# Kernel tuning notes

Hardware: AMD Instinct MI355X
Metric: run time of the kernel (lower is better)

The kernel has to match this reference:

```python
import jax, jax.numpy as jnp
import numpy as np
import math

NQ = 8            # n_qubits (hardcoded in _TransformerBlockQuantum)
DIM = 2 ** NQ     # statevector size = 256
H = 16            # num_heads
EPS = 1e-5        # LayerNorm eps

# PauliZ expectation table: wire 0 = most significant bit. ZTAB[w, j] = +/-1
_bits = (np.arange(DIM)[None, :] >> (NQ - 1 - np.arange(NQ)[:, None])) & 1
ZTAB = (1.0 - 2.0 * _bits).astype(np.float32)  # [NQ, DIM]


def _apply_1q(state, gate, w):
    # state: [N, 2^NQ] complex, gate: [N, 2, 2] complex, acts on wire w (MSB ordering)
    N = state.shape[0]
    s = state.reshape(N, 2 ** w, 2, 2 ** (NQ - w - 1))
    s = jnp.einsum('nab,npbq->npaq', gate, s)
    return s.reshape(N, DIM)


def _apply_cnot(state, c):
    # CNOT with control wire c, target wire c+1 (adjacent chain)
    N = state.shape[0]
    s = state.reshape(N, 2 ** c, 2, 2, 2 ** (NQ - c - 2))
    s = jnp.concatenate([s[:, :, :1], jnp.flip(s[:, :, 1:], axis=3)], axis=2)
    return s.reshape(N, DIM)


def _layernorm(x, g, b):
    mu = jnp.mean(x, axis=-1, keepdims=True)
    var = jnp.mean((x - mu) ** 2, axis=-1, keepdims=True)
    return (x - mu) / jnp.sqrt(var + EPS) * g + b


def _quantum_ffn(x, Win, b_in, Wout, b_out, ry):
    B, S, D = x.shape
    ang = (jnp.einsum('bsd,qd->bsq', x, Win) + b_in).reshape(-1, NQ)  # [N, NQ]
    N = ang.shape[0]
    state = jnp.zeros((N, DIM), jnp.complex64).at[:, 0].set(1.0)
    # RX encoding (per-token angles)
    for w in range(NQ):
        th = ang[:, w] * 0.5
        c, s = jnp.cos(th), jnp.sin(th)
        g = jnp.stack([jnp.stack([c, -1j * s], -1), jnp.stack([-1j * s, c], -1)], -2)
        state = _apply_1q(state, g.astype(jnp.complex64), w)
    # trainable RY (shared angles)
    for w in range(NQ):
        th = ry[w] * 0.5
        c, s = jnp.cos(th), jnp.sin(th)
        g = jnp.stack([jnp.stack([c, -s]), jnp.stack([s, c])]).astype(jnp.complex64)
        state = _apply_1q(state, jnp.broadcast_to(g, (N, 2, 2)), w)
    # CNOT entangling chain
    for w in range(NQ - 1):
        state = _apply_cnot(state, w)
    probs = jnp.abs(state) ** 2                      # [N, DIM] float32
    expz = probs @ ZTAB.T                            # [N, NQ]
    out = jnp.einsum('bsq,dq->bsd', expz.reshape(B, S, NQ), Wout) + b_out
    return jax.nn.relu(out)  # dropout = identity in eval


def _forward(x, Wq, Wk, Wv, Wo, g1, b1, g2, b2, Win, b_in, Wout, b_out, ry):
    B, S, D = x.shape
    dk = D // H
    q = jnp.einsum('bsd,ed->bse', x, Wq).reshape(B, S, H, dk)
    k = jnp.einsum('bsd,ed->bse', x, Wk).reshape(B, S, H, dk)
    v = jnp.einsum('bsd,ed->bse', x, Wv).reshape(B, S, H, dk)
    scores = jnp.einsum('bqhd,bkhd->bhqk', q, k) / math.sqrt(dk)
    attn = jax.nn.softmax(scores, axis=-1)
    o = jnp.einsum('bhqk,bkhd->bqhd', attn, v).reshape(B, S, D)
    attn_out = jnp.einsum('bsd,ed->bse', o, Wo)
    x1 = _layernorm(x + attn_out, g1, b1)
    ffn_out = _quantum_ffn(x1, Win, b_in, Wout, b_out, ry)
    return _layernorm(x1 + ffn_out, g2, b2)


def setup_inputs() -> dict:
    key = jax.random.key(0)
    ks = jax.random.split(key, 16)
    B, S, D = 2, 2048, 1024
    sd = 1.0 / math.sqrt(D)
    return {
        'x': jax.random.normal(ks[0], (B, S, D), jnp.float32),
        'Wq': jax.random.normal(ks[1], (D, D), jnp.float32) * sd,
        'Wk': jax.random.normal(ks[2], (D, D), jnp.float32) * sd,
        'Wv': jax.random.normal(ks[3], (D, D), jnp.float32) * sd,
        'Wo': jax.random.normal(ks[4], (D, D), jnp.float32) * sd,
        'g1': jnp.ones((D,), jnp.float32),
        'b1': jnp.zeros((D,), jnp.float32),
        'g2': jnp.ones((D,), jnp.float32),
        'b2': jnp.zeros((D,), jnp.float32),
        'Win': jax.random.normal(ks[5], (NQ, D), jnp.float32) * sd,
        'b_in': jnp.zeros((NQ,), jnp.float32),
        'Wout': jax.random.normal(ks[6], (D, NQ), jnp.float32) * (1.0 / math.sqrt(NQ)),
        'b_out': jnp.zeros((D,), jnp.float32),
        'ry': jax.random.normal(ks[7], (NQ,), jnp.float32) * 0.1,
    }


def reference(x, Wq, Wk, Wv, Wo, g1, b1, g2, b2, Win, b_in, Wout, b_out, ry):
    return _forward(x, Wq, Wk, Wv, Wo, g1, b1, g2, b2, Win, b_in, Wout, b_out, ry)
```

## Files before the change

### kernel.cpp

```cpp
#include <hip/hip_runtime.h>
#include <stdint.h>


typedef unsigned short u16;
typedef unsigned int   u32;
typedef __bf16 bf16x8 __attribute__((ext_vector_type(8)));
typedef u16    u16x8  __attribute__((ext_vector_type(8)));
typedef u16    u16x4  __attribute__((ext_vector_type(4)));
typedef float  f32x4  __attribute__((ext_vector_type(4)));
typedef float  f32x16 __attribute__((ext_vector_type(16)));

#define DEV static __device__ __forceinline__

DEV u16 f2b(float f){ u32 u = __float_as_uint(f); return (u16)((u + 0x7fffu + ((u>>16)&1u)) >> 16); }
DEV u16 b2u(__bf16 h){ union{__bf16 b; u16 u;} c; c.b = h; return c.u; }
DEV float exp2fast(float x){ return __builtin_amdgcn_exp2f(x); }

DEV void plswap(u32 a, u32 b, u32& o0, u32& o1, int hi){
#if __has_builtin(__builtin_amdgcn_permlane32_swap)
  auto s = __builtin_amdgcn_permlane32_swap(a, b, false, false);
  o0 = s[0]; o1 = s[1];
#else
  u32 xa = __shfl_xor(a, 32), xb = __shfl_xor(b, 32);
  o0 = hi ? xb : a;
  o1 = hi ? b  : xa;
#endif
}

#define MFMA16(a,b,c) __builtin_amdgcn_mfma_f32_16x16x32_bf16((a),(b),(c),0,0,0)
#define MFMA32(a,b,c) __builtin_amdgcn_mfma_f32_32x32x16_bf16((a),(b),(c),0,0,0)
#define GLD16(gp,lp) __builtin_amdgcn_global_load_lds( \
    (const __attribute__((address_space(1))) u32*)(const void*)(gp), \
    (__attribute__((address_space(3))) u32*)(void*)(lp), 16, 0, 0)

__global__ __launch_bounds__(256) void k_cast(const float* __restrict__ src, u16* __restrict__ dst){
  const int i = blockIdx.x*256 + threadIdx.x;
  const f32x4* s = (const f32x4*)src + (size_t)i*2;
  f32x4 a = s[0], b = s[1];
  u16x8 o;
  o[0]=f2b(a.x); o[1]=f2b(a.y); o[2]=f2b(a.z); o[3]=f2b(a.w);
  o[4]=f2b(b.x); o[5]=f2b(b.y); o[6]=f2b(b.z); o[7]=f2b(b.w);
  ((u16x8*)dst)[i] = o;
}

__global__ __launch_bounds__(256) void k_cast_w(
    const float* __restrict__ Wq, const float* __restrict__ Wk,
    const float* __restrict__ Wv, const float* __restrict__ Wo,
    u16* __restrict__ wb, u16* __restrict__ wob){
  const int r = blockIdx.x >> 9, bi = blockIdx.x & 511;
  const float* src = (r==0)?Wq:((r==1)?Wk:((r==2)?Wv:Wo));
  u16* dst = (r<3) ? (wb + (size_t)r*1048576) : wob;
  const int i = bi*256 + threadIdx.x;
  const f32x4* s = (const f32x4*)src + (size_t)i*2;
  f32x4 a = s[0], b = s[1];
  u16x8 o;
  o[0]=f2b(a.x); o[1]=f2b(a.y); o[2]=f2b(a.z); o[3]=f2b(a.w);
  o[4]=f2b(b.x); o[5]=f2b(b.y); o[6]=f2b(b.z); o[7]=f2b(b.w);
  ((u16x8*)dst)[i] = o;
}

template<int MODE>
__global__ __launch_bounds__(256) void k_gemm_nt(
    const u16* __restrict__ A, const u16* __restrict__ B,
    float* __restrict__ Cf, u16* __restrict__ Qo, u16* __restrict__ Ko, u16* __restrict__ Vt,
    int K, int N)
{
  __shared__ __attribute__((aligned(16))) u16 As[128*64];
  __shared__ __attribute__((aligned(16))) u16 Bs[128*64];
  const int tid = threadIdx.x, lane = tid & 63, w = tid >> 6;
  const int wr = w >> 1, wc = w & 1;
  const int nwg = gridDim.x * gridDim.y;
  int lin = blockIdx.y * gridDim.x + blockIdx.x;
  lin = (lin & 7) * (nwg >> 3) + (lin >> 3);
  const int n0 = (lin % gridDim.x) * 128;
  const int m0 = (lin / gridDim.x) * 128;
  const int l15 = lane & 15, lg = lane >> 4;
  f32x4 acc[4][4] = {};
  const int lr = lane >> 3, lc = (lane & 7)*8;
  const u16* ag = A + (size_t)(m0 + w*32 + lr)*K + lc;
  const u16* bg = B + (size_t)(n0 + w*32 + lr)*K + lc;
  u16* asl = &As[(w*32)*64];
  u16* bsl = &Bs[(w*32)*64];
  for (int k0 = 0; k0 < K; k0 += 64){
    __syncthreads();
    #pragma unroll
    for (int c = 0; c < 4; ++c){
      GLD16(ag + (size_t)(c*8)*K + k0, asl + c*512);
      GLD16(bg + (size_t)(c*8)*K + k0, bsl + c*512);
    }
    __syncthreads();
    #pragma unroll
    for (int kk = 0; kk < 2; ++kk){
      const int ko = kk*32 + lg*8;
      bf16x8 af[4], bf[4];
      #pragma unroll
      for (int t=0;t<4;++t) af[t] = *(const bf16x8*)&As[(wr*64 + t*16 + l15)*64 + ko];
      #pragma unroll
      for (int t=0;t<4;++t) bf[t] = *(const bf16x8*)&Bs[(wc*64 + t*16 + l15)*64 + ko];
      #pragma unroll
      for (int i=0;i<4;++i)
        #pragma unroll
        for (int j=0;j<4;++j)
          acc[i][j] = MFMA16(af[i], bf[j], acc[i][j]);
    }
  }
  const int col0 = n0 + wc*64 + l15;
  const int row0 = m0 + wr*64 + lg*4;
  if (MODE==0){
    const int which = n0 >> 10;
    if (which == 2){
      #pragma unroll
      for (int i=0;i<4;++i){
        const int rr0 = row0 + i*16;
        const int bsel = rr0 >> 11, ss = rr0 & 2047;
        #pragma unroll
        for (int j=0;j<4;++j){
          const int d_loc = (col0 + j*16) & 1023;
          const int hh = d_loc >> 6, dd = d_loc & 63;
          u16x4 pk;
          #pragma unroll
          for (int r=0;r<4;++r) pk[r] = f2b(acc[i][j][r]);
          *(u16x4*)(Vt + ((size_t)((bsel*16 + hh)*64 + dd))*2048 + ss) = pk;
        }
      }
    } else {
      u16* dst = which ? Ko : Qo;
      const float scl = which ? 1.f : 0.125f*1.44269504f;
      #pragma unroll
      for (int i=0;i<4;++i)
      #pragma unroll
      for (int j=0;j<4;++j){
        const int cc = (col0 + j*16) & 1023;
        #pragma unroll
        for (int r=0;r<4;++r)
          dst[(size_t)(row0 + i*16 + r)*1024 + cc] = f2b(acc[i][j][r]*scl);
      }
    }
  } else {
    #pragma unroll
    for (int i=0;i<4;++i)
    #pragma unroll
    for (int j=0;j<4;++j){
      const int cc = col0 + j*16;
      #pragma unroll
      for (int r=0;r<4;++r)
        Cf[(size_t)(row0 + i*16 + r)*N + cc] = acc[i][j][r];
    }
  }
}

__global__ __launch_bounds__(512) void k_attn(
    const u16* __restrict__ q, const u16* __restrict__ k,
    const u16* __restrict__ vt, u16* __restrict__ o)
{
  __shared__ __attribute__((aligned(16))) char KVb[65536];
  const int tid = threadIdx.x, lane = tid & 63;
  const int wl = (tid >> 6) & 3, wg = tid >> 8;
  const int p = blockIdx.x >> 4, qt = blockIdx.x & 15;
  const int b = p >> 4, h = p & 15;
  const int l31 = lane & 31, hi = lane >> 5;
  const int qrow = b*2048 + qt*128 + wl*32 + l31;
  const int swz = (l31 & 7) << 4;
  bf16x8 qa[4];
  #pragma unroll
  for (int kk=0;kk<4;++kk)
    qa[kk] = *(const bf16x8*)(q + (size_t)qrow*1024 + h*64 + kk*16 + hi*8);
  const char* kgl[2]; const char* vgl[2];
  #pragma unroll
  for (int i=0;i<2;++i){
    const int s = wl*2048 + i*1024 + lane*16;
    const int row = s >> 7;
    const int cb = (s & 127) ^ ((row & 7) << 4);
    kgl[i] = (const char*)k  + ((size_t)(b*2048 + wg*1024 + row))*2048 + h*128 + cb;
    vgl[i] = (const char*)vt + ((size_t)(p*64 + row))*4096 + wg*2048 + cb;
  }
  const int gbase = wg*32768;
  f32x16 oacc[2] = {};
  float mrow = -1e30f, lrow = 0.f;
  #pragma unroll
  for (int i=0;i<2;++i){
    GLD16(kgl[i], KVb + gbase + wl*2048 + i*1024);
    GLD16(vgl[i], KVb + gbase + 8192 + wl*2048 + i*1024);
  }
  for (int it = 0; it < 16; ++it){
    __syncthreads();
    if (it < 15){
      const size_t nkv = (size_t)(it+1)*64;
      const int nb = gbase + (((it+1)&1)<<14);
      #pragma unroll
      for (int i=0;i<2;++i){
        GLD16(kgl[i] + nkv*2048, KVb + nb + wl*2048 + i*1024);
        GLD16(vgl[i] + nkv*2,    KVb + nb + 8192 + wl*2048 + i*1024);
      }
    }
    const char* Kb = KVb + gbase + ((it&1)<<14);
    const char* Vb = Kb + 8192;
    f32x16 sacc[2] = {};
    __builtin_amdgcn_s_setprio(1);
    #pragma unroll
    for (int t32=0;t32<2;++t32){
      const int row = t32*32 + l31;
      #pragma unroll
      for (int kk=0;kk<4;++kk){
        bf16x8 kf = *(const bf16x8*)(Kb + row*128 + ((kk*32 + hi*16) ^ swz));
        sacc[t32] = MFMA32(kf, qa[kk], sacc[t32]);
      }
    }
    __builtin_amdgcn_s_setprio(0);
    float mx = sacc[0][0];
    #pragma unroll
    for (int t32=0;t32<2;++t32)
      #pragma unroll
      for (int i=0;i<16;++i) mx = fmaxf(mx, sacc[t32][i]);
    mx = fmaxf(mx, __shfl_xor(mx, 32));
    if (!__all(mx <= mrow + 8.f)){
      const float mnew = fmaxf(mrow, mx);
      const float scl = exp2fast(mrow - mnew);
      mrow = mnew; lrow *= scl;
      #pragma unroll
      for (int dt=0;dt<2;++dt)
        #pragma unroll
        for (int i=0;i<16;++i) oacc[dt][i] *= scl;
    }
    float rsum = 0.f;
    #pragma unroll
    for (int t32=0;t32<2;++t32)
      #pragma unroll
      for (int i=0;i<16;++i){
        const float e = exp2fast(sacc[t32][i] - mrow);
        sacc[t32][i] = e; rsum += e;
      }
    rsum += __shfl_xor(rsum, 32);
    lrow += rsum;
    u32 pk[2][8];
    #pragma unroll
    for (int t32=0;t32<2;++t32)
      #pragma unroll
      for (int u=0;u<8;++u){
        const int idx = (u>>1)*4 + (u&1)*2;
        const u32 lo = b2u((__bf16)sacc[t32][idx]);
        const u32 hh = b2u((__bf16)sacc[t32][idx+1]);
        pk[t32][u] = lo | (hh << 16);
      }
    bf16x8 pb[4];
    #pragma unroll
    for (int op=0;op<4;++op){
      const int t32 = op>>1, base = (op&1)*4;
      u32 w0,w1,w2,w3;
      plswap(pk[t32][base+0], pk[t32][base+2], w0, w2, hi);
      plswap(pk[t32][base+1], pk[t32][base+3], w1, w3, hi);
      union { u32 u[4]; bf16x8 v; } cc;
      cc.u[0]=w0; cc.u[1]=w1; cc.u[2]=w2; cc.u[3]=w3;
      pb[op] = cc.v;
    }
    __builtin_amdgcn_s_setprio(1);
    #pragma unroll
    for (int dt=0;dt<2;++dt){
      const int row = dt*32 + l31;
      #pragma unroll
      for (int op=0;op<4;++op){
        bf16x8 vf = *(const bf16x8*)(Vb + row*128 + ((op*32 + hi*16) ^ swz));
        oacc[dt] = MFMA32(vf, pb[op], oacc[dt]);
      }
    }
    __builtin_amdgcn_s_setprio(0);
  }
  __syncthreads();
  char* OB = KVb + 32768;
  char* MLB = KVb + 49152;
  if (wg == 1){
    #pragma unroll
    for (int dt=0;dt<2;++dt)
    #pragma unroll
    for (int rg=0;rg<4;++rg)
    #pragma unroll
    for (int hf=0;hf<2;++hf){
      const int r0 = rg*4 + hf*2;
      const u32 lo = b2u((__bf16)oacc[dt][r0]);
      const u32 hh = b2u((__bf16)oacc[dt][r0+1]);
      const int j = dt*8 + rg*2 + hf;
      *(u32*)(OB + wl*4096 + j*256 + lane*4) = lo | (hh << 16);
    }
    if (hi == 0)
      *(float2*)(MLB + (wl*32 + l31)*8) = make_float2(mrow, lrow);
  }
  __syncthreads();
  if (wg == 0){
    const float2 ml1 = *(const float2*)(MLB + (wl*32 + l31)*8);
    const float m  = fmaxf(mrow, ml1.x);
    const float a0 = exp2fast(mrow - m), a1 = exp2fast(ml1.x - m);
    const float linv = 1.f / (lrow*a0 + ml1.y*a1);
    const float s0 = a0*linv, s1 = a1*linv;
    u16* orow = o + (size_t)qrow*1024 + h*64;
    #pragma unroll
    for (int dt=0;dt<2;++dt)
    #pragma unroll
    for (int rg=0;rg<4;++rg)
    #pragma unroll
    for (int hf=0;hf<2;++hf){
      const int r0 = rg*4 + hf*2;
      const int j = dt*8 + rg*2 + hf;
      const u32 pu = *(const u32*)(OB + wl*4096 + j*256 + lane*4);
      const float p0 = __uint_as_float(pu << 16);
      const float p1 = __uint_as_float(pu & 0xFFFF0000u);
      const float v0 = oacc[dt][r0]  *s0 + p0*s1;
      const float v1 = oacc[dt][r0+1]*s0 + p1*s1;
      *(u32*)(orow + dt*32 + rg*8 + hi*4 + hf*2) = (u32)b2u((__bf16)v0) | ((u32)b2u((__bf16)v1) << 16);
    }
  }
}

__global__ __launch_bounds__(256) void k_tail(
    const float* __restrict__ x, const float* __restrict__ attn,
    const float* __restrict__ g1, const float* __restrict__ b1,
    const float* __restrict__ Win, const float* __restrict__ b_in,
    const float* __restrict__ Wout, const float* __restrict__ b_out,
    const float* __restrict__ ry,
    const float* __restrict__ g2, const float* __restrict__ b2,
    float* __restrict__ out)
{
  const int tid = threadIdx.x, lane = tid & 63, w = tid >> 6;
  const int t = blockIdx.x*4 + w;
  const size_t base = (size_t)t*1024;
  f32x4 yv[4];
  float s1 = 0.f, s2 = 0.f;
  #pragma unroll
  for (int c=0;c<4;++c){
    const int idx = c*256 + lane*4;
    f32x4 xv = *(const f32x4*)(x + base + idx);
    f32x4 av = *(const f32x4*)(attn + base + idx);
    f32x4 y = xv + av;
    yv[c] = y;
    s1 += y.x + y.y + y.z + y.w;
    s2 += y.x*y.x + y.y*y.y + y.z*y.z + y.w*y.w;
  }
  #pragma unroll
  for (int off=32; off; off>>=1){ s1 += __shfl_xor(s1, off); s2 += __shfl_xor(s2, off); }
  {
    const float mu = s1*(1.f/1024.f);
    const float rinv = rsqrtf(s2*(1.f/1024.f) - mu*mu + 1e-5f);
    #pragma unroll
    for (int c=0;c<4;++c){
      const int idx = c*256 + lane*4;
      f32x4 gv = *(const f32x4*)(g1 + idx);
      f32x4 bv = *(const f32x4*)(b1 + idx);
      f32x4 y = yv[c];
      y.x = (y.x-mu)*rinv*gv.x + bv.x;
      y.y = (y.y-mu)*rinv*gv.y + bv.y;
      y.z = (y.z-mu)*rinv*gv.z + bv.z;
      y.w = (y.w-mu)*rinv*gv.w + bv.w;
      yv[c] = y;
    }
  }
  float ang[8];
  #pragma unroll
  for (int qq=0; qq<8; ++qq){
    float acc = 0.f;
    #pragma unroll
    for (int c=0;c<4;++c){
      f32x4 wv = *(const f32x4*)(Win + qq*1024 + c*256 + lane*4);
      acc += wv.x*yv[c].x + wv.y*yv[c].y + wv.z*yv[c].z + wv.w*yv[c].w;
    }
    ang[qq] = acc;
  }
  #pragma unroll
  for (int off=32; off; off>>=1)
    #pragma unroll
    for (int qq=0; qq<8; ++qq) ang[qq] += __shfl_xor(ang[qq], off);
  #pragma unroll
  for (int qq=0; qq<8; ++qq) ang[qq] += b_in[qq];
  float vr[4], vi[4];
  #pragma unroll
  for (int r=0;r<4;++r){ vr[r]=0.f; vi[r]=0.f; }
  if (lane==0) vr[0] = 1.f;
  #pragma unroll
  for (int wi=0; wi<8; ++wi){
    float s, c; __sincosf(ang[wi]*0.5f, &s, &c);
    const int pbit = 7 - wi;
    if (pbit >= 6){
      const int rp = 1 << (pbit-6);
      #pragma unroll
      for (int r=0;r<4;++r) if (!(r & rp)){
        const int r2 = r | rp;
        float ar=vr[r], ai=vi[r], br=vr[r2], bi=vi[r2];
        vr[r]  = c*ar + s*bi;  vi[r]  = c*ai - s*br;
        vr[r2] = c*br + s*ai;  vi[r2] = c*bi - s*ar;
      }
    } else {
      const int msk = 1 << pbit;
      #pragma unroll
      for (int r=0;r<4;++r){
        float orr = __shfl_xor(vr[r], msk);
        float oii = __shfl_xor(vi[r], msk);
        float nr = c*vr[r] + s*oii;
        float ni = c*vi[r] - s*orr;
        vr[r]=nr; vi[r]=ni;
      }
    }
  }
  #pragma unroll
  for (int wi=0; wi<8; ++wi){
    float s, c; __sincosf(ry[wi]*0.5f, &s, &c);
    const int pbit = 7 - wi;
    if (pbit >= 6){
      const int rp = 1 << (pbit-6);
      #pragma unroll
      for (int r=0;r<4;++r) if (!(r & rp)){
        const int r2 = r | rp;
        float ar=vr[r], ai=vi[r], br=vr[r2], bi=vi[r2];
        vr[r]  = c*ar - s*br;  vi[r]  = c*ai - s*bi;
        vr[r2] = s*ar + c*br;  vi[r2] = s*ai + c*bi;
      }
    } else {
      const int msk = 1 << pbit;
      const float sg = (lane & msk) ? s : -s;
      #pragma unroll
      for (int r=0;r<4;++r){
        float orr = __shfl_xor(vr[r], msk);
        float oii = __shfl_xor(vi[r], msk);
        float nr = c*vr[r] + sg*orr;
        float ni = c*vi[r] + sg*oii;
        vr[r]=nr; vi[r]=ni;
      }
    }
  }
  { float tr=vr[2]; vr[2]=vr[3]; vr[3]=tr; float ti=vi[2]; vi[2]=vi[3]; vi[3]=ti; }
  vr[1]=__shfl_xor(vr[1],32); vi[1]=__shfl_xor(vi[1],32);
  vr[3]=__shfl_xor(vr[3],32); vi[3]=__shfl_xor(vi[3],32);
  #pragma unroll
  for (int cn=2; cn<7; ++cn){
    const int pc = 7-cn, pt = pc-1;
    const bool ctl = (lane >> pc) & 1;
    #pragma unroll
    for (int r=0;r<4;++r){
      float tr = __shfl_xor(vr[r], 1<<pt);
      float ti = __shfl_xor(vi[r], 1<<pt);
      if (ctl){ vr[r]=tr; vi[r]=ti; }
    }
  }
  float pr[4];
  #pragma unroll
  for (int r=0;r<4;++r) pr[r] = vr[r]*vr[r] + vi[r]*vi[r];
  float e[8];
  e[0] = (pr[0]+pr[1]) - (pr[2]+pr[3]);
  e[1] = (pr[0]+pr[2]) - (pr[1]+pr[3]);
  const float tot = pr[0]+pr[1]+pr[2]+pr[3];
  #pragma unroll
  for (int wi=2; wi<8; ++wi){
    const int pbit = 7-wi;
    e[wi] = ((lane >> pbit) & 1) ? -tot : tot;
  }
  #pragma unroll
  for (int off=1; off<64; off<<=1)
    #pragma unroll
    for (int i=0;i<8;++i) e[i] += __shfl_xor(e[i], off);
  float yy[4][4];
  s1 = 0.f; s2 = 0.f;
  #pragma unroll
  for (int c=0;c<4;++c){
    const float x1a[4] = {yv[c].x, yv[c].y, yv[c].z, yv[c].w};
    #pragma unroll
    for (int j=0;j<4;++j){
      const int d = c*256 + lane*4 + j;
      f32x4 w0 = *(const f32x4*)(Wout + (size_t)d*8);
      f32x4 w1 = *(const f32x4*)(Wout + (size_t)d*8 + 4);
      float acc = b_out[d];
      acc += w0.x*e[0] + w0.y*e[1] + w0.z*e[2] + w0.w*e[3];
      acc += w1.x*e[4] + w1.y*e[5] + w1.z*e[6] + w1.w*e[7];
      const float y = x1a[j] + fmaxf(acc, 0.f);
      yy[c][j] = y;
      s1 += y; s2 += y*y;
    }
  }
  #pragma unroll
  for (int off=32; off; off>>=1){ s1 += __shfl_xor(s1, off); s2 += __shfl_xor(s2, off); }
  const float mu = s1*(1.f/1024.f);
  const float rinv = rsqrtf(s2*(1.f/1024.f) - mu*mu + 1e-5f);
  #pragma unroll
  for (int c=0;c<4;++c){
    const int idx = c*256 + lane*4;
    f32x4 gv = *(const f32x4*)(g2 + idx);
    f32x4 bv = *(const f32x4*)(b2 + idx);
    f32x4 ov;
    ov.x = (yy[c][0]-mu)*rinv*gv.x + bv.x;
    ov.y = (yy[c][1]-mu)*rinv*gv.y + bv.y;
    ov.z = (yy[c][2]-mu)*rinv*gv.z + bv.z;
    ov.w = (yy[c][3]-mu)*rinv*gv.w + bv.w;
    *(f32x4*)(out + base + idx) = ov;
  }
}

extern "C" void kernel_launch(void* const* d_in, const int* in_sizes, int n_in,
                              void* d_out, int out_size, void* d_ws, size_t ws_size,
                              hipStream_t stream)
{
  const float* x    = (const float*)d_in[0];
  const float* Wq   = (const float*)d_in[1];
  const float* Wk   = (const float*)d_in[2];
  const float* Wv   = (const float*)d_in[3];
  const float* Wo   = (const float*)d_in[4];
  const float* g1   = (const float*)d_in[5];
  const float* b1   = (const float*)d_in[6];
  const float* g2   = (const float*)d_in[7];
  const float* b2   = (const float*)d_in[8];
  const float* Win  = (const float*)d_in[9];
  const float* b_in = (const float*)d_in[10];
  const float* Wout = (const float*)d_in[11];
  const float* b_out= (const float*)d_in[12];
  const float* ry   = (const float*)d_in[13];
  float* out = (float*)d_out;
  char* ws = (char*)d_ws;
  const size_t MB = 1024u*1024u;
  u16* xb  = (u16*)(ws + 0*MB);
  u16* wb  = (u16*)(ws + 8*MB);
  u16* wob = (u16*)(ws + 14*MB);
  u16* qb  = (u16*)(ws + 16*MB);
  u16* kb  = (u16*)(ws + 24*MB);
  u16* vtb = (u16*)(ws + 32*MB);
  u16* ob  = (u16*)(ws + 40*MB);
  float* attn_out = (float*)(ws + 48*MB);

  k_cast<<<2048, 256, 0, stream>>>(x, xb);
  k_cast_w<<<2048, 256, 0, stream>>>(Wq, Wk, Wv, Wo, wb, wob);
  k_gemm_nt<0><<<dim3(24,32), 256, 0, stream>>>(xb, wb, nullptr, qb, kb, vtb, 1024, 3072);
  k_attn<<<512, 512, 0, stream>>>(qb, kb, vtb, ob);
  k_gemm_nt<1><<<dim3(8,32), 256, 0, stream>>>(ob, wob, attn_out, nullptr, nullptr, nullptr, 1024, 1024);
  k_tail<<<1024, 256, 0, stream>>>(x, attn_out, g1, b1, Win, b_in, Wout, b_out, ry, g2, b2, out);
}
```

Before: 266.4 us.

## Load K/V fragments directly from global memory in attention, dropping LDS staging

The attention kernel no longer stages K and V tiles through double-buffered shared memory with async global-to-LDS copies and per-iteration barriers. Each wave now reads its K and V MFMA fragments straight from global memory into registers, and the V loads are issued before the softmax so their latency can overlap it. LDS use shrinks to the output-combine buffers, which may raise occupancy and removes the in-loop syncs. In exchange, K/V reuse across the four waves of a group now comes only from cache rather than LDS, so global and L2 traffic goes up and load latency is exposed more.

```diff
diff --git a/kernel.cpp b/kernel.cpp
--- a/kernel.cpp
+++ b/kernel.cpp
@@ -153,60 +153,44 @@
     const u16* __restrict__ q, const u16* __restrict__ k,
     const u16* __restrict__ vt, u16* __restrict__ o)
 {
-  __shared__ __attribute__((aligned(16))) char KVb[65536];
+  __shared__ __attribute__((aligned(16))) char OB[16384];
+  __shared__ __attribute__((aligned(16))) char MLB[1024];
   const int tid = threadIdx.x, lane = tid & 63;
   const int wl = (tid >> 6) & 3, wg = tid >> 8;
   const int p = blockIdx.x >> 4, qt = blockIdx.x & 15;
   const int b = p >> 4, h = p & 15;
   const int l31 = lane & 31, hi = lane >> 5;
   const int qrow = b*2048 + qt*128 + wl*32 + l31;
-  const int swz = (l31 & 7) << 4;
   bf16x8 qa[4];
   #pragma unroll
   for (int kk=0;kk<4;++kk)
     qa[kk] = *(const bf16x8*)(q + (size_t)qrow*1024 + h*64 + kk*16 + hi*8);
-  const char* kgl[2]; const char* vgl[2];
-  #pragma unroll
-  for (int i=0;i<2;++i){
-    const int s = wl*2048 + i*1024 + lane*16;
-    const int row = s >> 7;
-    const int cb = (s & 127) ^ ((row & 7) << 4);
-    kgl[i] = (const char*)k  + ((size_t)(b*2048 + wg*1024 + row))*2048 + h*128 + cb;
-    vgl[i] = (const char*)vt + ((size_t)(p*64 + row))*4096 + wg*2048 + cb;
-  }
-  const int gbase = wg*32768;
+  const u16* kbase = k + (size_t)(b*2048 + wg*1024 + l31)*1024 + h*64 + hi*8;
+  const u16* vbase = vt + (size_t)(p*64 + l31)*2048 + wg*1024 + hi*8;
   f32x16 oacc[2] = {};
   float mrow = -1e30f, lrow = 0.f;
-  #pragma unroll
-  for (int i=0;i<2;++i){
-    GLD16(kgl[i], KVb + gbase + wl*2048 + i*1024);
-    GLD16(vgl[i], KVb + gbase + 8192 + wl*2048 + i*1024);
-  }
   for (int it = 0; it < 16; ++it){
-    __syncthreads();
-    if (it < 15){
-      const size_t nkv = (size_t)(it+1)*64;
-      const int nb = gbase + (((it+1)&1)<<14);
-      #pragma unroll
-      for (int i=0;i<2;++i){
-        GLD16(kgl[i] + nkv*2048, KVb + nb + wl*2048 + i*1024);
-        GLD16(vgl[i] + nkv*2,    KVb + nb + 8192 + wl*2048 + i*1024);
-      }
-    }
-    const char* Kb = KVb + gbase + ((it&1)<<14);
-    const char* Vb = Kb + 8192;
+    const u16* kp = kbase + (size_t)(it*64)*1024;
+    const u16* vp = vbase + it*64;
     f32x16 sacc[2] = {};
-    __builtin_amdgcn_s_setprio(1);
     #pragma unroll
     for (int t32=0;t32<2;++t32){
-      const int row = t32*32 + l31;
-      #pragma unroll
-      for (int kk=0;kk<4;++kk){
-        bf16x8 kf = *(const bf16x8*)(Kb + row*128 + ((kk*32 + hi*16) ^ swz));
-        sacc[t32] = MFMA32(kf, qa[kk], sacc[t32]);
-      }
-    }
-    __builtin_amdgcn_s_setprio(0);
+      bf16x8 kf[4];
+      #pragma unroll
+      for (int kk=0;kk<4;++kk)
+        kf[kk] = *(const bf16x8*)(kp + (size_t)(t32*32)*1024 + kk*16);
+      __builtin_amdgcn_s_setprio(1);
+      #pragma unroll
+      for (int kk=0;kk<4;++kk)
+        sacc[t32] = MFMA32(kf[kk], qa[kk], sacc[t32]);
+      __builtin_amdgcn_s_setprio(0);
+    }
+    bf16x8 vf[2][4];
+    #pragma unroll
+    for (int dt=0;dt<2;++dt)
+      #pragma unroll
+      for (int op=0;op<4;++op)
+        vf[dt][op] = *(const bf16x8*)(vp + (size_t)(dt*32)*2048 + op*16);
     float mx = sacc[0][0];
     #pragma unroll
     for (int t32=0;t32<2;++t32)
@@ -255,19 +239,13 @@
     }
     __builtin_amdgcn_s_setprio(1);
     #pragma unroll
-    for (int dt=0;dt<2;++dt){
-      const int row = dt*32 + l31;
-      #pragma unroll
-      for (int op=0;op<4;++op){
-        bf16x8 vf = *(const bf16x8*)(Vb + row*128 + ((op*32 + hi*16) ^ swz));
-        oacc[dt] = MFMA32(vf, pb[op], oacc[dt]);
-      }
-    }
+    for (int dt=0;dt<2;++dt)
+      #pragma unroll
+      for (int op=0;op<4;++op)
+        oacc[dt] = MFMA32(vf[dt][op], pb[op], oacc[dt]);
     __builtin_amdgcn_s_setprio(0);
   }
   __syncthreads();
-  char* OB = KVb + 32768;
-  char* MLB = KVb + 49152;
   if (wg == 1){
     #pragma unroll
     for (int dt=0;dt<2;++dt)
```

Measured after the change: 328.3 us. 1.23x slower.
